# Kernel optimization log

Hardware: AMD Instinct MI355X
Metric: run time of the kernel (lower is better)

## Reference

```python
import jax, jax.numpy as jnp
import numpy as np

WS = 8          # window size
HEADS = 6
DIM = 192


def _rel_idx(ws):
    # index [q, k] -> flat relative-position index into table of size (2ws-1)^2
    pos = jnp.arange(ws * ws)
    ph, pw = pos // ws, pos % ws
    rel_h = ph[None, :] - ph[:, None] + ws - 1  # k_h - q_h + ws - 1
    rel_w = pw[None, :] - pw[:, None] + ws - 1
    return rel_h * (2 * ws - 1) + rel_w  # [ws*ws, ws*ws]


def setup_inputs() -> dict:
    key = jax.random.key(0)
    ks = jax.random.split(key, 4)
    x = jax.random.normal(ks[0], (4, DIM, 256, 256), jnp.float32)
    qkv_w = jax.random.normal(ks[1], (3 * DIM, DIM), jnp.float32) * 0.02  # 1x1 conv
    qkv_b = jnp.zeros((3 * DIM,), jnp.float32)
    out_w = jax.random.normal(ks[2], (DIM, DIM), jnp.float32) * 0.02      # 1x1 conv
    out_b = jnp.zeros((DIM,), jnp.float32)
    rpe_table = jax.random.normal(ks[3], (HEADS, (2 * WS - 1) ** 2), jnp.float32) * 0.001
    return {"x": x, "qkv_w": qkv_w, "qkv_b": qkv_b,
            "out_w": out_w, "out_b": out_b, "rpe_table": rpe_table}


def reference(x, qkv_w, qkv_b, out_w, out_b, rpe_table):
    B, C, H, W = x.shape
    ws, heads = WS, HEADS
    hd, wd = H // ws, W // ws          # H,W chosen divisible by ws -> pad is no-op
    c = C // heads                     # head dim
    n = ws * ws                        # tokens per window

    # 1x1 conv to qkv
    qkv = jnp.einsum('bchw,oc->bohw', x, qkv_w) + qkv_b[None, :, None, None]
    # feat_to_win: b (3 heads c) (hd ws) (wd ws) -> 3, (b hd wd), heads, n, c
    qkv = qkv.reshape(B, 3, heads, c, hd, ws, wd, ws)
    qkv = qkv.transpose(1, 0, 4, 6, 2, 5, 7, 3).reshape(3, B * hd * wd, heads, n, c)
    q, k, v = qkv[0], qkv[1], qkv[2]

    bias = rpe_table[:, _rel_idx(ws)]  # [heads, n, n]
    scale = c ** -0.5
    scores = jnp.einsum('whqc,whkc->whqk', q, k) * scale + bias[None]
    attn = jax.nn.softmax(scores, axis=-1)
    out = jnp.einsum('whqk,whkc->whqc', attn, v)

    # win_to_feat: (b hd wd) heads n c -> b (heads c) H W
    out = out.reshape(B, hd, wd, heads, ws, ws, c)
    out = out.transpose(0, 3, 6, 1, 4, 2, 5).reshape(B, C, H, W)

    out = jnp.einsum('bchw,oc->bohw', out, out_w) + out_b[None, :, None, None]
    return out
```

## Files before the change

kernel.cpp:

```cpp
#include <hip/hip_runtime.h>
#include <cstdint>
#include <cstddef>

typedef __attribute__((ext_vector_type(8))) short short8;
typedef __attribute__((ext_vector_type(4))) float floatx4;
typedef __attribute__((ext_vector_type(16))) float floatx16;

#define SEG 50331648ull

__device__ __forceinline__ unsigned short bf16rne(float f) {
  union { float f; unsigned int u; } c; c.f = f;
  unsigned int u = c.u;
  return (unsigned short)((u + 0x7fffu + ((u >> 16) & 1u)) >> 16);
}
__device__ __forceinline__ unsigned int packbf(float a, float b) {
  return (unsigned int)bf16rne(a) | ((unsigned int)bf16rne(b) << 16);
}
__device__ __forceinline__ unsigned int cvtpk(float lo, float hi) {
  unsigned int r;
  asm("v_cvt_pk_bf16_f32 %0, %1, %2" : "=v"(r) : "v"(lo), "v"(hi));
  return r;
}

__global__ __launch_bounds__(256) void x_to_bf16(const float* __restrict__ x,
                                                 unsigned short* __restrict__ xb) {
  __shared__ float Tl[64][65];
  const int tid = threadIdx.x;
  const int ptile = blockIdx.x, cc = blockIdx.y, b = blockIdx.z;
  const float* src = x + ((size_t)(b * 192 + cc * 64)) * 65536 + ptile * 64;
  {
    int row = tid >> 2;
    int cb = (tid & 3) * 4;
#pragma unroll
    for (int rr = 0; rr < 4; ++rr) {
      int col = cb + rr * 16;
      float4 v = *(const float4*)(src + (size_t)row * 65536 + col);
      *(float4*)&Tl[row][col] = v;
    }
  }
  __syncthreads();
  unsigned short* dst = xb + ((size_t)b * 65536 + (size_t)ptile * 64) * 192 + cc * 64;
  {
    int p_l = tid >> 2;
    int c0 = (tid & 3) * 16;
    unsigned int w[8];
#pragma unroll
    for (int e = 0; e < 8; ++e)
      w[e] = packbf(Tl[c0 + 2 * e][p_l], Tl[c0 + 2 * e + 1][p_l]);
    *(uint4*)(dst + (size_t)p_l * 192 + c0)     = make_uint4(w[0], w[1], w[2], w[3]);
    *(uint4*)(dst + (size_t)p_l * 192 + c0 + 8) = make_uint4(w[4], w[5], w[6], w[7]);
  }
}

__global__ void bias_prep(const float* __restrict__ rpe, float* __restrict__ bias_d) {
  const int head = blockIdx.x;
  const int tid = threadIdx.x;
  for (int e = tid; e < 4096; e += 256) {
    int f = e >> 10;
    int lane = (e >> 4) & 63;
    int reg = e & 15;
    int kt2 = f >> 1, qt2 = f & 1;
    int qq = qt2 * 32 + (lane & 31);
    int kk = kt2 * 32 + (reg & 3) + 8 * (reg >> 2) + 4 * (lane >> 5);
    int idx = ((kk >> 3) - (qq >> 3) + 7) * 15 + ((kk & 7) - (qq & 7) + 7);
    bias_d[((size_t)(head * 4 + f) * 64 + lane) * 16 + reg] = rpe[head * 225 + idx];
  }
}

#define WP 200
#define XP 200
__global__ __launch_bounds__(256) void qkv_mm(
    const unsigned short* __restrict__ xb, const float* __restrict__ wq,
    const float* __restrict__ qkv_b,
    unsigned short* __restrict__ q, unsigned short* __restrict__ k,
    unsigned short* __restrict__ v) {
  __shared__ unsigned short Xl[128 * XP];
  __shared__ unsigned short Wl[64 * WP];
  const int tid = threadIdx.x;
  const int pt = blockIdx.x, b = blockIdx.y;
  const int lane = tid & 63, w = tid >> 6;
  const int n16 = lane & 15, quad = lane >> 4;

  const unsigned short* xrow = xb + ((size_t)b * 65536 + (size_t)pt * 128) * 192;
#pragma unroll
  for (int r = 0; r < 12; ++r) {
    int c = tid + 256 * r;
    int row = c / 24;
    int col = (c - row * 24) * 8;
    short8 xv = *(const short8*)(xrow + (size_t)c * 8);
    *(short8*)&Xl[row * XP + col] = xv;
  }
  const int wo = tid >> 2, wcb = (tid & 3) * 4;
  float4 wpre[12];
#pragma unroll
  for (int r = 0; r < 12; ++r)
    wpre[r] = *(const float4*)(wq + (size_t)wo * 192 + wcb + r * 16);
#pragma unroll
  for (int r = 0; r < 12; ++r)
    *(uint2*)&Wl[wo * WP + wcb + r * 16] =
        make_uint2(packbf(wpre[r].x, wpre[r].y), packbf(wpre[r].z, wpre[r].w));
  __syncthreads();

  const floatx4 fz = {0.f, 0.f, 0.f, 0.f};
#pragma unroll 1
  for (int ot = 0; ot < 9; ++ot) {
    if (ot < 8) {
      const float* wr = wq + (size_t)((ot + 1) * 64 + wo) * 192 + wcb;
#pragma unroll
      for (int r = 0; r < 12; ++r) wpre[r] = *(const float4*)(wr + r * 16);
    }
    floatx4 acc[4][2];
#pragma unroll
    for (int i = 0; i < 4; ++i)
#pragma unroll
      for (int j = 0; j < 2; ++j) acc[i][j] = fz;
#pragma unroll
    for (int k0 = 0; k0 < 192; k0 += 32) {
      short8 a[4], bf[2];
#pragma unroll
      for (int i = 0; i < 4; ++i)
        a[i] = *(const short8*)&Wl[(16 * i + n16) * WP + k0 + quad * 8];
#pragma unroll
      for (int j = 0; j < 2; ++j)
        bf[j] = *(const short8*)&Xl[(w * 32 + 16 * j + n16) * XP + k0 + quad * 8];
#pragma unroll
      for (int i = 0; i < 4; ++i)
#pragma unroll
        for (int j = 0; j < 2; ++j)
          acc[i][j] = __builtin_amdgcn_mfma_f32_16x16x32_bf16(a[i], bf[j], acc[i][j], 0, 0, 0);
    }
    __syncthreads();
    if (ot < 8) {
#pragma unroll
      for (int r = 0; r < 12; ++r)
        *(uint2*)&Wl[wo * WP + wcb + r * 16] =
            make_uint2(packbf(wpre[r].x, wpre[r].y), packbf(wpre[r].z, wpre[r].w));
    }
    __syncthreads();

    const int sel = ot / 3;
    unsigned short* dst = (sel == 0) ? q : ((sel == 1) ? k : v);
    const float scl = (sel == 0) ? 0.17677669529663687f : 1.0f;
    const int h = pt >> 1;
#pragma unroll
    for (int j = 0; j < 2; ++j) {
      int wcol = w * 32 + 16 * j + n16;
      int wc = ((pt & 1) << 7) + wcol;
      int win = (b << 10) + (h >> 3) * 32 + (wc >> 3);
      int t = ((h & 7) << 3) + (wc & 7);
#pragma unroll
      for (int i = 0; i < 4; ++i) {
        int og = ot * 64 + 16 * i + quad * 4;
        int off = og - sel * 192;
        int head = off >> 5, c = off & 31;
        float4 bb = *(const float4*)(qkv_b + og);
        float v0 = (acc[i][j][0] + bb.x) * scl;
        float v1 = (acc[i][j][1] + bb.y) * scl;
        float v2 = (acc[i][j][2] + bb.z) * scl;
        float v3 = (acc[i][j][3] + bb.w) * scl;
        *(uint2*)(dst + ((size_t)(win * 6 + head) * 64 + t) * 32 + c) =
            make_uint2(packbf(v0, v1), packbf(v2, v3));
      }
    }
  }
}

__global__ __launch_bounds__(256) void attn(
    const unsigned short* __restrict__ q, const unsigned short* __restrict__ k,
    const unsigned short* __restrict__ v, const float* __restrict__ bias_d,
    unsigned short* __restrict__ AO) {
  __shared__ unsigned short vl[4][32 * 72];
  const int tid = threadIdx.x, w = tid >> 6, lane = tid & 63;
  const int m32 = lane & 31, half = lane >> 5;
  const int wh = blockIdx.x * 4 + w;
  const int win = wh / 6, head = wh - win * 6;
  const unsigned short* qb = q + (size_t)wh * 2048;
  const unsigned short* kb = k + (size_t)wh * 2048;
  const unsigned short* vb = v + (size_t)wh * 2048;

  short8 vrow[4];
#pragma unroll
  for (int c8 = 0; c8 < 4; ++c8)
    vrow[c8] = *(const short8*)(vb + lane * 32 + c8 * 8);

  short8 ka[2][2];
#pragma unroll
  for (int kt2 = 0; kt2 < 2; ++kt2)
#pragma unroll
    for (int cc = 0; cc < 2; ++cc)
      ka[kt2][cc] = *(const short8*)(kb + (size_t)(kt2 * 32 + m32) * 32 + cc * 16 + half * 8);

  unsigned short* vlw = (unsigned short*)vl[w];
#pragma unroll
  for (int c8 = 0; c8 < 4; ++c8)
#pragma unroll
    for (int e = 0; e < 8; ++e)
      vlw[(c8 * 8 + e) * 72 + lane] = (unsigned short)vrow[c8][e];

  short8 va[4];
#pragma unroll
  for (int k16 = 0; k16 < 4; ++k16)
    va[k16] = *(const short8*)&vlw[m32 * 72 + k16 * 16 + half * 8];

  const float* bD = bias_d + (size_t)head * 4096;
  const floatx16 fz16 = {0.f,0.f,0.f,0.f,0.f,0.f,0.f,0.f,0.f,0.f,0.f,0.f,0.f,0.f,0.f,0.f};

#pragma unroll
  for (int qt2 = 0; qt2 < 2; ++qt2) {
    float4 bb[8];
#pragma unroll
    for (int g = 0; g < 4; ++g)
      bb[g] = *(const float4*)(bD + ((size_t)(qt2 * 64) + lane) * 16 + g * 4);
#pragma unroll
    for (int g = 0; g < 4; ++g)
      bb[4 + g] = *(const float4*)(bD + ((size_t)((2 + qt2) * 64) + lane) * 16 + g * 4);

    short8 qf0 = *(const short8*)(qb + (size_t)(qt2 * 32 + m32) * 32 + half * 8);
    short8 qf1 = *(const short8*)(qb + (size_t)(qt2 * 32 + m32) * 32 + 16 + half * 8);

    floatx16 st0 = __builtin_amdgcn_mfma_f32_32x32x16_bf16(ka[0][0], qf0, fz16, 0, 0, 0);
    st0 = __builtin_amdgcn_mfma_f32_32x32x16_bf16(ka[0][1], qf1, st0, 0, 0, 0);
    floatx16 st1 = __builtin_amdgcn_mfma_f32_32x32x16_bf16(ka[1][0], qf0, fz16, 0, 0, 0);
    st1 = __builtin_amdgcn_mfma_f32_32x32x16_bf16(ka[1][1], qf1, st1, 0, 0, 0);

    float x[32];
#pragma unroll
    for (int r = 0; r < 16; ++r) x[r]      = st0[r] + ((const float*)&bb[r >> 2])[r & 3];
#pragma unroll
    for (int r = 0; r < 16; ++r) x[16 + r] = st1[r] + ((const float*)&bb[4 + (r >> 2)])[r & 3];

    float mx = x[0];
#pragma unroll
    for (int r = 1; r < 32; ++r) mx = fmaxf(mx, x[r]);
    mx = fmaxf(mx, __shfl_xor(mx, 32));
    float s = 0.f;
#pragma unroll
    for (int r = 0; r < 32; ++r) { x[r] = __expf(x[r] - mx); s += x[r]; }
    s += __shfl_xor(s, 32);
    float iv = 1.0f / s;

    unsigned int u[16];
#pragma unroll
    for (int j = 0; j < 16; ++j) u[j] = cvtpk(x[2 * j], x[2 * j + 1]);

    floatx16 o = fz16;
#pragma unroll
    for (int k16 = 0; k16 < 4; ++k16) {
      int base = (k16 >> 1) * 8 + (k16 & 1) * 4;
      unsigned int a0 = u[base + 0], b0 = u[base + 2];
      unsigned int a1 = u[base + 1], b1 = u[base + 3];
      asm("v_permlane32_swap_b32 %0, %1" : "+v"(a0), "+v"(b0));
      asm("v_permlane32_swap_b32 %0, %1" : "+v"(a1), "+v"(b1));
      union { unsigned int wd[4]; short8 s8; } bw;
      bw.wd[0] = a0; bw.wd[1] = a1; bw.wd[2] = b0; bw.wd[3] = b1;
      o = __builtin_amdgcn_mfma_f32_32x32x16_bf16(va[k16], bw.s8, o, 0, 0, 0);
    }

    const int t = qt2 * 32 + m32;
    const int bimg = win >> 10, rem = win & 1023;
    const int h0 = (rem >> 5) << 3, w0 = (rem & 31) << 3;
    const size_t pix = ((size_t)bimg << 16) + (size_t)(h0 + (t >> 3)) * 256 + w0 + (t & 7);
    unsigned short* dstp = AO + pix * 192 + head * 32 + half * 4;
#pragma unroll
    for (int g = 0; g < 4; ++g) {
      float v0 = o[4 * g + 0] * iv, v1 = o[4 * g + 1] * iv;
      float v2 = o[4 * g + 2] * iv, v3 = o[4 * g + 3] * iv;
      *(uint2*)(dstp + g * 8) = make_uint2(cvtpk(v0, v1), cvtpk(v2, v3));
    }
  }
}

__global__ __launch_bounds__(256) void out_mm(
    const unsigned short* __restrict__ AO, const float* __restrict__ w2,
    const float* __restrict__ b2, float* __restrict__ out) {
  __shared__ unsigned short Xl[128 * XP];
  __shared__ unsigned short Wl[64 * WP];
  const int tid = threadIdx.x;
  const int pt = blockIdx.x, b = blockIdx.y;
  const int lane = tid & 63, w = tid >> 6;
  const int n16 = lane & 15, quad = lane >> 4;

  const unsigned short* arow = AO + ((size_t)b * 65536 + (size_t)pt * 128) * 192;
#pragma unroll
  for (int r = 0; r < 12; ++r) {
    int c = tid + 256 * r;
    int row = c / 24;
    int col = (c - row * 24) * 8;
    short8 xv = *(const short8*)(arow + (size_t)c * 8);
    *(short8*)&Xl[row * XP + col] = xv;
  }
  const int wo = tid >> 2, wcb = (tid & 3) * 4;
  float4 wpre[12];
#pragma unroll
  for (int r = 0; r < 12; ++r)
    wpre[r] = *(const float4*)(w2 + (size_t)wo * 192 + wcb + r * 16);
#pragma unroll
  for (int r = 0; r < 12; ++r)
    *(uint2*)&Wl[wo * WP + wcb + r * 16] =
        make_uint2(packbf(wpre[r].x, wpre[r].y), packbf(wpre[r].z, wpre[r].w));
  __syncthreads();

  const floatx4 fz = {0.f, 0.f, 0.f, 0.f};
#pragma unroll 1
  for (int ot = 0; ot < 3; ++ot) {
    if (ot < 2) {
      const float* wr = w2 + (size_t)((ot + 1) * 64 + wo) * 192 + wcb;
#pragma unroll
      for (int r = 0; r < 12; ++r) wpre[r] = *(const float4*)(wr + r * 16);
    }
    floatx4 acc[2][4];
#pragma unroll
    for (int i = 0; i < 2; ++i)
#pragma unroll
      for (int j = 0; j < 4; ++j) acc[i][j] = fz;
#pragma unroll
    for (int k0 = 0; k0 < 192; k0 += 32) {
      short8 a[2], bf[4];
#pragma unroll
      for (int i = 0; i < 2; ++i)
        a[i] = *(const short8*)&Xl[(w * 32 + 16 * i + n16) * XP + k0 + quad * 8];
#pragma unroll
      for (int j = 0; j < 4; ++j)
        bf[j] = *(const short8*)&Wl[(16 * j + n16) * WP + k0 + quad * 8];
#pragma unroll
      for (int i = 0; i < 2; ++i)
#pragma unroll
        for (int j = 0; j < 4; ++j)
          acc[i][j] = __builtin_amdgcn_mfma_f32_16x16x32_bf16(a[i], bf[j], acc[i][j], 0, 0, 0);
    }
    __syncthreads();
    if (ot < 2) {
#pragma unroll
      for (int r = 0; r < 12; ++r)
        *(uint2*)&Wl[wo * WP + wcb + r * 16] =
            make_uint2(packbf(wpre[r].x, wpre[r].y), packbf(wpre[r].z, wpre[r].w));
    }
    __syncthreads();

#pragma unroll
    for (int j = 0; j < 4; ++j) {
      int o = ot * 64 + 16 * j + n16;
      float bj = b2[o];
      float* obase = out + ((size_t)b * 192 + o) * 65536 + (size_t)pt * 128;
#pragma unroll
      for (int i = 0; i < 2; ++i) {
        int p = w * 32 + 16 * i + quad * 4;
        *(float4*)(obase + p) = make_float4(acc[i][j][0] + bj, acc[i][j][1] + bj,
                                            acc[i][j][2] + bj, acc[i][j][3] + bj);
      }
    }
  }
}

extern "C" void kernel_launch(void* const* d_in, const int* in_sizes, int n_in,
                              void* d_out, int out_size, void* d_ws, size_t ws_size,
                              hipStream_t stream) {
  const float* x     = (const float*)d_in[0];
  const float* qkv_w = (const float*)d_in[1];
  const float* qkv_b = (const float*)d_in[2];
  const float* out_w = (const float*)d_in[3];
  const float* out_b = (const float*)d_in[4];
  const float* rpe   = (const float*)d_in[5];
  float* out = (float*)d_out;

  unsigned short* xb = (unsigned short*)d_ws;
  unsigned short* q  = xb + SEG;
  unsigned short* k  = q + SEG;
  unsigned short* v  = k + SEG;
  unsigned short* AO = v + SEG;
  float* bias_d = (float*)(AO + SEG);

  x_to_bf16<<<dim3(1024, 3, 4), 256, 0, stream>>>(x, xb);
  bias_prep<<<6, 256, 0, stream>>>(rpe, bias_d);
  qkv_mm<<<dim3(512, 4), 256, 0, stream>>>(xb, qkv_w, qkv_b, q, k, v);
  attn<<<6144, 256, 0, stream>>>(q, k, v, bias_d, AO);
  out_mm<<<dim3(512, 4), 256, 0, stream>>>(AO, out_w, out_b, out);
}
```

Baseline: 666.7 us.

## Fuse x fp32-to-bf16 transpose into qkv GEMM and pre-convert weights once

Drops the separate x_to_bf16 pass. The qkv GEMM now loads fp32 x tiles directly, transposes them through shared memory and converts to bf16 in place, which avoids writing and re-reading a full bf16 copy of x. A small w_prep kernel converts the qkv and out weights to bf16 once, folds the q scale into the weights and bias, and lets both GEMMs load bf16 weights with short8 loads. The cost is a longer prologue in qkv_mm, with six shared-memory transpose rounds and extra barriers before the MFMA loop. Rounding also differs slightly because the scale is applied before the bf16 cast.

```diff
diff --git a/kernel.cpp b/kernel.cpp
--- a/kernel.cpp
+++ b/kernel.cpp
@@ -22,33 +22,22 @@
   return r;
 }
 
-__global__ __launch_bounds__(256) void x_to_bf16(const float* __restrict__ x,
-                                                 unsigned short* __restrict__ xb) {
-  __shared__ float Tl[64][65];
-  const int tid = threadIdx.x;
-  const int ptile = blockIdx.x, cc = blockIdx.y, b = blockIdx.z;
-  const float* src = x + ((size_t)(b * 192 + cc * 64)) * 65536 + ptile * 64;
-  {
-    int row = tid >> 2;
-    int cb = (tid & 3) * 4;
-#pragma unroll
-    for (int rr = 0; rr < 4; ++rr) {
-      int col = cb + rr * 16;
-      float4 v = *(const float4*)(src + (size_t)row * 65536 + col);
-      *(float4*)&Tl[row][col] = v;
-    }
-  }
-  __syncthreads();
-  unsigned short* dst = xb + ((size_t)b * 65536 + (size_t)ptile * 64) * 192 + cc * 64;
-  {
-    int p_l = tid >> 2;
-    int c0 = (tid & 3) * 16;
-    unsigned int w[8];
-#pragma unroll
-    for (int e = 0; e < 8; ++e)
-      w[e] = packbf(Tl[c0 + 2 * e][p_l], Tl[c0 + 2 * e + 1][p_l]);
-    *(uint4*)(dst + (size_t)p_l * 192 + c0)     = make_uint4(w[0], w[1], w[2], w[3]);
-    *(uint4*)(dst + (size_t)p_l * 192 + c0 + 8) = make_uint4(w[4], w[5], w[6], w[7]);
+__global__ __launch_bounds__(256) void w_prep(
+    const float* __restrict__ wq, const float* __restrict__ qb,
+    const float* __restrict__ ow,
+    unsigned short* __restrict__ wqb, unsigned short* __restrict__ owb,
+    float* __restrict__ qbs) {
+  const float S = 0.17677669529663687f;
+  int id = blockIdx.x * 256 + threadIdx.x;
+  if (id < 55296) {
+    float s = (id < 18432) ? S : 1.0f;
+    ((unsigned int*)wqb)[id] = packbf(wq[2 * id] * s, wq[2 * id + 1] * s);
+  } else if (id < 55296 + 18432) {
+    int j = id - 55296;
+    ((unsigned int*)owb)[j] = packbf(ow[2 * j], ow[2 * j + 1]);
+  } else if (id < 55296 + 18432 + 576) {
+    int j = id - 55296 - 18432;
+    qbs[j] = qb[j] * (j < 192 ? S : 1.0f);
   }
 }
 
@@ -70,44 +59,66 @@
 #define WP 200
 #define XP 200
 __global__ __launch_bounds__(256) void qkv_mm(
-    const unsigned short* __restrict__ xb, const float* __restrict__ wq,
-    const float* __restrict__ qkv_b,
+    const float* __restrict__ x, const unsigned short* __restrict__ wqb,
+    const float* __restrict__ qbs,
     unsigned short* __restrict__ q, unsigned short* __restrict__ k,
     unsigned short* __restrict__ v) {
   __shared__ unsigned short Xl[128 * XP];
-  __shared__ unsigned short Wl[64 * WP];
+  __shared__ union UB { unsigned short Wl[64 * WP]; float Tl[64][65]; } U;
   const int tid = threadIdx.x;
   const int pt = blockIdx.x, b = blockIdx.y;
   const int lane = tid & 63, w = tid >> 6;
   const int n16 = lane & 15, quad = lane >> 4;
 
-  const unsigned short* xrow = xb + ((size_t)b * 65536 + (size_t)pt * 128) * 192;
-#pragma unroll
-  for (int r = 0; r < 12; ++r) {
-    int c = tid + 256 * r;
-    int row = c / 24;
-    int col = (c - row * 24) * 8;
-    short8 xv = *(const short8*)(xrow + (size_t)c * 8);
-    *(short8*)&Xl[row * XP + col] = xv;
-  }
-  const int wo = tid >> 2, wcb = (tid & 3) * 4;
-  float4 wpre[12];
-#pragma unroll
-  for (int r = 0; r < 12; ++r)
-    wpre[r] = *(const float4*)(wq + (size_t)wo * 192 + wcb + r * 16);
-#pragma unroll
-  for (int r = 0; r < 12; ++r)
-    *(uint2*)&Wl[wo * WP + wcb + r * 16] =
-        make_uint2(packbf(wpre[r].x, wpre[r].y), packbf(wpre[r].z, wpre[r].w));
+  {
+    const float* xbase = x + (size_t)b * 192 * 65536 + (size_t)pt * 128;
+    const int row = tid >> 2, cb = (tid & 3) * 4;
+    const int p_l = tid >> 2, c0 = (tid & 3) * 16;
+#pragma unroll 1
+    for (int tile = 0; tile < 6; ++tile) {
+      int cc = tile >> 1, ph = tile & 1;
+      const float* src = xbase + (size_t)(cc * 64 + row) * 65536 + ph * 64;
+#pragma unroll
+      for (int rr = 0; rr < 4; ++rr) {
+        int col = cb + rr * 16;
+        *(float4*)&U.Tl[row][col] = *(const float4*)(src + col);
+      }
+      __syncthreads();
+      unsigned int wd[8];
+#pragma unroll
+      for (int e = 0; e < 8; ++e)
+        wd[e] = cvtpk(U.Tl[c0 + 2 * e][p_l], U.Tl[c0 + 2 * e + 1][p_l]);
+      unsigned short* xd = &Xl[(ph * 64 + p_l) * XP + cc * 64];
+      *(uint4*)(xd + c0)     = make_uint4(wd[0], wd[1], wd[2], wd[3]);
+      *(uint4*)(xd + c0 + 8) = make_uint4(wd[4], wd[5], wd[6], wd[7]);
+      __syncthreads();
+    }
+  }
+
+  int wrow[6], wcol[6];
+#pragma unroll
+  for (int r = 0; r < 6; ++r) {
+    int id = tid + 256 * r;
+    wrow[r] = id / 24;
+    wcol[r] = (id - wrow[r] * 24) * 8;
+  }
+  short8 wpre[6];
+#pragma unroll
+  for (int r = 0; r < 6; ++r)
+    wpre[r] = *(const short8*)(wqb + (size_t)wrow[r] * 192 + wcol[r]);
+#pragma unroll
+  for (int r = 0; r < 6; ++r)
+    *(short8*)&U.Wl[wrow[r] * WP + wcol[r]] = wpre[r];
   __syncthreads();
 
   const floatx4 fz = {0.f, 0.f, 0.f, 0.f};
 #pragma unroll 1
   for (int ot = 0; ot < 9; ++ot) {
     if (ot < 8) {
-      const float* wr = wq + (size_t)((ot + 1) * 64 + wo) * 192 + wcb;
-#pragma unroll
-      for (int r = 0; r < 12; ++r) wpre[r] = *(const float4*)(wr + r * 16);
+      const unsigned short* wn = wqb + (size_t)(ot + 1) * 64 * 192;
+#pragma unroll
+      for (int r = 0; r < 6; ++r)
+        wpre[r] = *(const short8*)(wn + (size_t)wrow[r] * 192 + wcol[r]);
     }
     floatx4 acc[4][2];
 #pragma unroll
@@ -119,7 +130,7 @@
       short8 a[4], bf[2];
 #pragma unroll
       for (int i = 0; i < 4; ++i)
-        a[i] = *(const short8*)&Wl[(16 * i + n16) * WP + k0 + quad * 8];
+        a[i] = *(const short8*)&U.Wl[(16 * i + n16) * WP + k0 + quad * 8];
 #pragma unroll
       for (int j = 0; j < 2; ++j)
         bf[j] = *(const short8*)&Xl[(w * 32 + 16 * j + n16) * XP + k0 + quad * 8];
@@ -132,20 +143,18 @@
     __syncthreads();
     if (ot < 8) {
 #pragma unroll
-      for (int r = 0; r < 12; ++r)
-        *(uint2*)&Wl[wo * WP + wcb + r * 16] =
-            make_uint2(packbf(wpre[r].x, wpre[r].y), packbf(wpre[r].z, wpre[r].w));
+      for (int r = 0; r < 6; ++r)
+        *(short8*)&U.Wl[wrow[r] * WP + wcol[r]] = wpre[r];
     }
     __syncthreads();
 
     const int sel = ot / 3;
     unsigned short* dst = (sel == 0) ? q : ((sel == 1) ? k : v);
-    const float scl = (sel == 0) ? 0.17677669529663687f : 1.0f;
     const int h = pt >> 1;
 #pragma unroll
     for (int j = 0; j < 2; ++j) {
-      int wcol = w * 32 + 16 * j + n16;
-      int wc = ((pt & 1) << 7) + wcol;
+      int wcol2 = w * 32 + 16 * j + n16;
+      int wc = ((pt & 1) << 7) + wcol2;
       int win = (b << 10) + (h >> 3) * 32 + (wc >> 3);
       int t = ((h & 7) << 3) + (wc & 7);
 #pragma unroll
@@ -153,13 +162,13 @@
         int og = ot * 64 + 16 * i + quad * 4;
         int off = og - sel * 192;
         int head = off >> 5, c = off & 31;
-        float4 bb = *(const float4*)(qkv_b + og);
-        float v0 = (acc[i][j][0] + bb.x) * scl;
-        float v1 = (acc[i][j][1] + bb.y) * scl;
-        float v2 = (acc[i][j][2] + bb.z) * scl;
-        float v3 = (acc[i][j][3] + bb.w) * scl;
+        float4 bb = *(const float4*)(qbs + og);
+        float v0 = acc[i][j][0] + bb.x;
+        float v1 = acc[i][j][1] + bb.y;
+        float v2 = acc[i][j][2] + bb.z;
+        float v3 = acc[i][j][3] + bb.w;
         *(uint2*)(dst + ((size_t)(win * 6 + head) * 64 + t) * 32 + c) =
-            make_uint2(packbf(v0, v1), packbf(v2, v3));
+            make_uint2(cvtpk(v0, v1), cvtpk(v2, v3));
       }
     }
   }
@@ -271,7 +280,7 @@
 }
 
 __global__ __launch_bounds__(256) void out_mm(
-    const unsigned short* __restrict__ AO, const float* __restrict__ w2,
+    const unsigned short* __restrict__ AO, const unsigned short* __restrict__ owb,
     const float* __restrict__ b2, float* __restrict__ out) {
   __shared__ unsigned short Xl[128 * XP];
   __shared__ unsigned short Wl[64 * WP];
@@ -289,24 +298,30 @@
     short8 xv = *(const short8*)(arow + (size_t)c * 8);
     *(short8*)&Xl[row * XP + col] = xv;
   }
-  const int wo = tid >> 2, wcb = (tid & 3) * 4;
-  float4 wpre[12];
-#pragma unroll
-  for (int r = 0; r < 12; ++r)
-    wpre[r] = *(const float4*)(w2 + (size_t)wo * 192 + wcb + r * 16);
-#pragma unroll
-  for (int r = 0; r < 12; ++r)
-    *(uint2*)&Wl[wo * WP + wcb + r * 16] =
-        make_uint2(packbf(wpre[r].x, wpre[r].y), packbf(wpre[r].z, wpre[r].w));
+  int wrow[6], wcol[6];
+#pragma unroll
+  for (int r = 0; r < 6; ++r) {
+    int id = tid + 256 * r;
+    wrow[r] = id / 24;
+    wcol[r] = (id - wrow[r] * 24) * 8;
+  }
+  short8 wpre[6];
+#pragma unroll
+  for (int r = 0; r < 6; ++r)
+    wpre[r] = *(const short8*)(owb + (size_t)wrow[r] * 192 + wcol[r]);
+#pragma unroll
+  for (int r = 0; r < 6; ++r)
+    *(short8*)&Wl[wrow[r] * WP + wcol[r]] = wpre[r];
   __syncthreads();
 
   const floatx4 fz = {0.f, 0.f, 0.f, 0.f};
 #pragma unroll 1
   for (int ot = 0; ot < 3; ++ot) {
     if (ot < 2) {
-      const float* wr = w2 + (size_t)((ot + 1) * 64 + wo) * 192 + wcb;
-#pragma unroll
-      for (int r = 0; r < 12; ++r) wpre[r] = *(const float4*)(wr + r * 16);
+      const unsigned short* wn = owb + (size_t)(ot + 1) * 64 * 192;
+#pragma unroll
+      for (int r = 0; r < 6; ++r)
+        wpre[r] = *(const short8*)(wn + (size_t)wrow[r] * 192 + wcol[r]);
     }
     floatx4 acc[2][4];
 #pragma unroll
@@ -331,9 +346,8 @@
     __syncthreads();
     if (ot < 2) {
 #pragma unroll
-      for (int r = 0; r < 12; ++r)
-        *(uint2*)&Wl[wo * WP + wcb + r * 16] =
-            make_uint2(packbf(wpre[r].x, wpre[r].y), packbf(wpre[r].z, wpre[r].w));
+      for (int r = 0; r < 6; ++r)
+        *(short8*)&Wl[wrow[r] * WP + wcol[r]] = wpre[r];
     }
     __syncthreads();
 
@@ -363,16 +377,18 @@
   const float* rpe   = (const float*)d_in[5];
   float* out = (float*)d_out;
 
-  unsigned short* xb = (unsigned short*)d_ws;
-  unsigned short* q  = xb + SEG;
+  unsigned short* wqb = (unsigned short*)d_ws;
+  unsigned short* owb = wqb + 110592;
+  float* qbs = (float*)(owb + 36864);
+  unsigned short* q  = (unsigned short*)d_ws + SEG;
   unsigned short* k  = q + SEG;
   unsigned short* v  = k + SEG;
   unsigned short* AO = v + SEG;
   float* bias_d = (float*)(AO + SEG);
 
-  x_to_bf16<<<dim3(1024, 3, 4), 256, 0, stream>>>(x, xb);
+  w_prep<<<291, 256, 0, stream>>>(qkv_w, qkv_b, out_w, wqb, owb, qbs);
   bias_prep<<<6, 256, 0, stream>>>(rpe, bias_d);
-  qkv_mm<<<dim3(512, 4), 256, 0, stream>>>(xb, qkv_w, qkv_b, q, k, v);
+  qkv_mm<<<dim3(512, 4), 256, 0, stream>>>(x, wqb, qbs, q, k, v);
   attn<<<6144, 256, 0, stream>>>(q, k, v, bias_d, AO);
-  out_mm<<<dim3(512, 4), 256, 0, stream>>>(AO, out_w, out_b, out);
-}
+  out_mm<<<dim3(512, 4), 256, 0, stream>>>(AO, owb, out_b, out);
+}
```

Result: faster. 648.0 us (-2.8%).
